# Performance work log

Hardware: AMD Instinct MI355X
Metric: run time of the kernel (lower is better)

## Reference

```python
import jax, jax.numpy as jnp
import numpy as np

N_NODES = 50000
N_EDGES = 800000
IN_F = 128
OUT_F = 128

def setup_inputs() -> dict:
    key = jax.random.key(0)
    k1, k2, k3, k4, k5, k6 = jax.random.split(key, 6)
    x = jax.random.normal(k1, (N_NODES, IN_F), dtype=jnp.float32)
    edge_row = jax.random.randint(k2, (N_EDGES,), 0, N_NODES, dtype=jnp.int32)
    edge_col = jax.random.randint(k3, (N_EDGES,), 0, N_NODES, dtype=jnp.int32)
    edge_val = jax.random.uniform(k4, (N_EDGES,), dtype=jnp.float32)
    stdv = 1.0 / np.sqrt(OUT_F)
    weight = jax.random.uniform(k5, (IN_F, OUT_F), minval=-stdv, maxval=stdv, dtype=jnp.float32)
    bias_param = jax.random.uniform(k6, (OUT_F,), minval=-stdv, maxval=stdv, dtype=jnp.float32)
    return {"x": x, "edge_row": edge_row, "edge_col": edge_col,
            "edge_val": edge_val, "weight": weight, "bias_param": bias_param}

def reference(x, edge_row, edge_col, edge_val, weight, bias_param):
    # support = X @ W  (dense GEMM)
    support = jnp.matmul(x, weight)                      # [N, out_f]
    # out = spmm(adj, support): gather source rows, scale by edge value,
    # scatter-add into destination rows (COO SpMM)
    msgs = edge_val[:, None] * support[edge_col]         # [E, out_f]
    out = jax.ops.segment_sum(msgs, edge_row, num_segments=N_NODES)
    return out + bias_param
```

## Files before the change

kernel.cpp:

```cpp
#include <hip/hip_runtime.h>

#define IN_F 128
#define OUT_F 128
#define BROWS 64
#define BCAP  2048
#define CHUNK 4096
#define NBMAX 1024

typedef __attribute__((ext_vector_type(8))) short short8;
typedef __attribute__((ext_vector_type(4))) float floatx4;

__device__ __forceinline__ short f2bf(float f) {
  union { float f; unsigned u; } v; v.f = f;
  unsigned u = v.u;
  unsigned r = (u + 0x7fffu + ((u >> 16) & 1u)) >> 16;
  return (short)r;
}
__device__ __forceinline__ float bflo(unsigned u) { return __uint_as_float(u << 16); }
__device__ __forceinline__ float bfhi(unsigned u) { return __uint_as_float(u & 0xffff0000u); }

__global__ __launch_bounds__(256) void prep_all(const float* __restrict__ w,
                                                short* __restrict__ wt,
                                                int* __restrict__ cursor, int nb) {
  int i = blockIdx.x * 256 + threadIdx.x;
  int n = i >> 7, k = i & 127;
  wt[i] = f2bf(w[k * 128 + n]);
  if (i < nb) cursor[i] = i * BCAP;
}

__global__ __launch_bounds__(256) void gemm_bin(const float* __restrict__ x,
                                                const short* __restrict__ wt,
                                                unsigned short* __restrict__ sup,
                                                const int* __restrict__ erow,
                                                const int* __restrict__ ecol,
                                                const float* __restrict__ eval_,
                                                int* __restrict__ cursor,
                                                int2* __restrict__ slab,
                                                int n_nodes, int n_edges,
                                                int nb, int n_tiles) {
  __shared__ __align__(16) unsigned short stile[4][16 * 136];
  __shared__ int lhist[NBMAX];
  const int t = threadIdx.x;

  if ((int)blockIdx.x < n_tiles) {
    const int wv   = t >> 6;
    const int lane = t & 63;
    const int m    = lane & 15;
    const int q    = lane >> 4;
    const int row  = blockIdx.x * 64 + wv * 16 + m;

    floatx4 acc[8];
#pragma unroll
    for (int k = 0; k < 8; ++k) acc[k] = (floatx4)(0.f);

#pragma unroll
    for (int kk = 0; kk < 4; ++kk) {
      short8 a;
      if (row < n_nodes) {
        const float4* px = (const float4*)(x + (size_t)row * IN_F + kk * 32 + q * 8);
        float4 lo = px[0], hi = px[1];
        a[0] = f2bf(lo.x); a[1] = f2bf(lo.y); a[2] = f2bf(lo.z); a[3] = f2bf(lo.w);
        a[4] = f2bf(hi.x); a[5] = f2bf(hi.y); a[6] = f2bf(hi.z); a[7] = f2bf(hi.w);
      } else {
        a = (short8)(0);
      }
#pragma unroll
      for (int k = 0; k < 8; ++k) {
        short8 b = *(const short8*)(wt + (size_t)(16 * k + m) * 128 + kk * 32 + q * 8);
        acc[k] = __builtin_amdgcn_mfma_f32_16x16x32_bf16(a, b, acc[k], 0, 0, 0);
      }
    }
#pragma unroll
    for (int r = 0; r < 4; ++r)
#pragma unroll
      for (int k = 0; k < 8; ++k)
        stile[wv][(q * 4 + r) * 136 + 16 * k + m] = (unsigned short)f2bf(acc[k][r]);
#pragma unroll
    for (int p = 0; p < 4; ++p) {
      int row_l = p * 4 + (lane >> 4);
      int row_g = blockIdx.x * 64 + wv * 16 + row_l;
      if (row_g < n_nodes) {
        uint4 v = *(const uint4*)&stile[wv][row_l * 136 + (lane & 15) * 8];
        *(uint4*)(sup + (size_t)row_g * OUT_F + (lane & 15) * 8) = v;
      }
    }
  } else {
    for (int b = t; b < nb; b += 256) lhist[b] = 0;
    __syncthreads();

    const int base = (blockIdx.x - n_tiles) * CHUNK;
    int meta[16], col[16]; float val[16];
#pragma unroll
    for (int i = 0; i < 16; ++i) {
      int e = base + i * 256 + t;
      meta[i] = -1;
      if (e < n_edges) {
        int r  = erow[e];
        col[i] = ecol[e];
        val[i] = eval_[e];
        int bk = r >> 6, rl = r & 63;
        int rank = atomicAdd(&lhist[bk], 1);
        meta[i] = (bk << 18) | (rl << 12) | rank;
      }
    }
    __syncthreads();
    for (int bk = t; bk < nb; bk += 256) {
      int c = lhist[bk];
      lhist[bk] = c ? atomicAdd(&cursor[bk], c) : 0;
    }
    __syncthreads();
#pragma unroll
    for (int i = 0; i < 16; ++i) {
      if (meta[i] >= 0) {
        int bk = meta[i] >> 18, rl = (meta[i] >> 12) & 63, rank = meta[i] & 0xfff;
        int pos = lhist[bk] + rank;
        if (pos < (bk + 1) * BCAP)
          slab[pos] = make_int2(col[i] | (rl << 16), __float_as_int(val[i]));
      }
    }
  }
}

__global__ __launch_bounds__(256) void spmm_sorted(const int* __restrict__ cursor,
                                                   const int2* __restrict__ slab,
                                                   const uint4* __restrict__ supv,
                                                   const float* __restrict__ bias,
                                                   float* __restrict__ out,
                                                   int n_nodes) {
  __shared__ int2 srec[BCAP];
  __shared__ int  roff[BROWS + 1];
  __shared__ int  rcur[BROWS];
  const int t = threadIdx.x, b = blockIdx.x;
  const int start = b * BCAP;
  const int cnt = min(cursor[b] - start, BCAP);
  const int wv = t >> 6, lane = t & 63;

  if (t < BROWS) rcur[t] = 0;
  __syncthreads();
  for (int i = t; i < cnt; i += 256)
    atomicAdd(&rcur[(slab[start + i].x >> 16) & 63], 1);
  __syncthreads();
  if (wv == 0) {
    int c = rcur[lane];
    int inc = c;
#pragma unroll
    for (int d = 1; d < 64; d <<= 1) {
      int u = __shfl_up(inc, d);
      if (lane >= d) inc += u;
    }
    roff[lane + 1] = inc;
    if (lane == 0) roff[0] = 0;
  }
  __syncthreads();
  if (t < BROWS) rcur[t] = roff[t];
  __syncthreads();
  for (int i = t; i < cnt; i += 256) {
    int2 r = slab[start + i];
    int p = atomicAdd(&rcur[(r.x >> 16) & 63], 1);
    srec[p] = r;
  }
  __syncthreads();

  const int g = lane >> 4, s = lane & 15;
  const float4* bp = (const float4*)bias + s * 2;
  const float4 b0 = bp[0], b1 = bp[1];

#pragma unroll
  for (int it = 0; it < 4; ++it) {
    const int rl = it * 16 + wv * 4 + g;
    const int s0 = roff[rl];
    const int c  = roff[rl + 1] - s0;
    int mx = max(c, __shfl_xor(c, 16));
    mx = max(mx, __shfl_xor(mx, 32));

    float a0 = 0.f, a1 = 0.f, a2 = 0.f, a3 = 0.f,
          a4 = 0.f, a5 = 0.f, a6 = 0.f, a7 = 0.f;

    int2  rec[4];
    uint4 sv[4];
#pragma unroll
    for (int k = 0; k < 4; ++k)
      rec[k] = (k < c) ? srec[s0 + k] : make_int2(0, 0);
#pragma unroll
    for (int k = 0; k < 4; ++k)
      sv[k] = supv[(size_t)(rec[k].x & 0xffff) * 16 + s];

    for (int j = 0; j < mx; j += 4) {
#pragma unroll
      for (int k = 0; k < 4; ++k) {
        const int jj = j + k;
        int2 recn = (jj + 4 < c) ? srec[s0 + jj + 4] : make_int2(0, 0);
        uint4 svn = supv[(size_t)(recn.x & 0xffff) * 16 + s];
        float v = (jj < c) ? __int_as_float(rec[k].y) : 0.f;
        a0 = fmaf(v, bflo(sv[k].x), a0);
        a1 = fmaf(v, bfhi(sv[k].x), a1);
        a2 = fmaf(v, bflo(sv[k].y), a2);
        a3 = fmaf(v, bfhi(sv[k].y), a3);
        a4 = fmaf(v, bflo(sv[k].z), a4);
        a5 = fmaf(v, bfhi(sv[k].z), a5);
        a6 = fmaf(v, bflo(sv[k].w), a6);
        a7 = fmaf(v, bfhi(sv[k].w), a7);
        rec[k] = recn; sv[k] = svn;
      }
    }

    const int row = b * BROWS + rl;
    if (row < n_nodes) {
      float4* op = (float4*)(out + (size_t)row * OUT_F + s * 8);
      op[0] = make_float4(a0 + b0.x, a1 + b0.y, a2 + b0.z, a3 + b0.w);
      op[1] = make_float4(a4 + b1.x, a5 + b1.y, a6 + b1.z, a7 + b1.w);
    }
  }
}

extern "C" void kernel_launch(void* const* d_in, const int* in_sizes, int n_in,
                              void* d_out, int out_size, void* d_ws, size_t ws_size,
                              hipStream_t stream) {
  const float* x     = (const float*)d_in[0];
  const int*   erow  = (const int*)d_in[1];
  const int*   ecol  = (const int*)d_in[2];
  const float* eval_ = (const float*)d_in[3];
  const float* w     = (const float*)d_in[4];
  const float* bias  = (const float*)d_in[5];
  float* out = (float*)d_out;

  const int n_nodes  = in_sizes[0] / IN_F;
  const int n_edges  = in_sizes[1];
  const int nb       = (n_nodes + BROWS - 1) / BROWS;
  const int n_tiles  = (n_nodes + 63) / 64;
  const int n_chunks = (n_edges + CHUNK - 1) / CHUNK;

  char* ws = (char*)d_ws;
  size_t off = 0;
  auto carve = [&](size_t bytes) { void* p = ws + off; off = (off + bytes + 255) & ~(size_t)255; return p; };
  unsigned short* sup = (unsigned short*)carve((size_t)n_nodes * OUT_F * sizeof(unsigned short));
  short* wt           = (short*)carve((size_t)IN_F * OUT_F * sizeof(short));
  int*   cursor       = (int*)  carve((size_t)nb * sizeof(int));
  int2*  slab         = (int2*) carve((size_t)nb * BCAP * sizeof(int2));

  prep_all<<<64, 256, 0, stream>>>(w, wt, cursor, nb);
  gemm_bin<<<n_tiles + n_chunks, 256, 0, stream>>>(x, wt, sup, erow, ecol, eval_,
                                                   cursor, slab, n_nodes, n_edges,
                                                   nb, n_tiles);
  spmm_sorted<<<nb, 256, 0, stream>>>(cursor, slab, (const uint4*)sup, bias, out, n_nodes);
}
```

Baseline: 138.4 us.

## Balance edge work across row groups via merge-path split in SpMM block

Each 16-lane group used to own fixed rows, so a wave's loop ran to the longest row among its groups. Now each of the 16 groups in the block takes an equal slice of the block's sorted edges, found by binary search over the row offsets. It walks those edges in order and flushes a row's result whenever a row boundary is crossed. This evens out load imbalance from varying row degrees, but adds data-dependent branches inside the inner loop and divergence within each wave.

```diff
diff --git a/kernel.cpp b/kernel.cpp
--- a/kernel.cpp
+++ b/kernel.cpp
@@ -161,17 +161,32 @@
   }
   __syncthreads();
 
-  const int g = lane >> 4, s = lane & 15;
+  const int gid = t >> 4;
+  const int s   = t & 15;
   const float4* bp = (const float4*)bias + s * 2;
   const float4 b0 = bp[0], b1 = bp[1];
-
-#pragma unroll
-  for (int it = 0; it < 4; ++it) {
-    const int rl = it * 16 + wv * 4 + g;
-    const int s0 = roff[rl];
-    const int c  = roff[rl + 1] - s0;
-    int mx = max(c, __shfl_xor(c, 16));
-    mx = max(mx, __shfl_xor(mx, 32));
+  const int row0 = b * BROWS;
+
+  int ra, rb;
+  {
+    int tgt = (gid * cnt) >> 4;
+    int lo = 0, hi = 64;
+    while (lo < hi) { int m = (lo + hi) >> 1; if (roff[m] >= tgt) hi = m; else lo = m + 1; }
+    ra = lo;
+    if (gid == 15) rb = 64;
+    else {
+      tgt = ((gid + 1) * cnt) >> 4;
+      lo = 0; hi = 64;
+      while (lo < hi) { int m = (lo + hi) >> 1; if (roff[m] >= tgt) hi = m; else lo = m + 1; }
+      rb = lo;
+    }
+  }
+
+  if (ra < rb) {
+    const int j0 = roff[ra];
+    const int j1 = roff[rb];
+    int cur  = ra;
+    int nend = roff[cur + 1];
 
     float a0 = 0.f, a1 = 0.f, a2 = 0.f, a3 = 0.f,
           a4 = 0.f, a5 = 0.f, a6 = 0.f, a7 = 0.f;
@@ -180,35 +195,49 @@
     uint4 sv[4];
 #pragma unroll
     for (int k = 0; k < 4; ++k)
-      rec[k] = (k < c) ? srec[s0 + k] : make_int2(0, 0);
+      rec[k] = (j0 + k < j1) ? srec[j0 + k] : make_int2(0, 0);
 #pragma unroll
     for (int k = 0; k < 4; ++k)
       sv[k] = supv[(size_t)(rec[k].x & 0xffff) * 16 + s];
 
-    for (int j = 0; j < mx; j += 4) {
+    for (int jb = j0; jb < j1; jb += 4) {
 #pragma unroll
       for (int k = 0; k < 4; ++k) {
-        const int jj = j + k;
-        int2 recn = (jj + 4 < c) ? srec[s0 + jj + 4] : make_int2(0, 0);
-        uint4 svn = supv[(size_t)(recn.x & 0xffff) * 16 + s];
-        float v = (jj < c) ? __int_as_float(rec[k].y) : 0.f;
-        a0 = fmaf(v, bflo(sv[k].x), a0);
-        a1 = fmaf(v, bfhi(sv[k].x), a1);
-        a2 = fmaf(v, bflo(sv[k].y), a2);
-        a3 = fmaf(v, bfhi(sv[k].y), a3);
-        a4 = fmaf(v, bflo(sv[k].z), a4);
-        a5 = fmaf(v, bfhi(sv[k].z), a5);
-        a6 = fmaf(v, bflo(sv[k].w), a6);
-        a7 = fmaf(v, bfhi(sv[k].w), a7);
-        rec[k] = recn; sv[k] = svn;
-      }
-    }
-
-    const int row = b * BROWS + rl;
-    if (row < n_nodes) {
-      float4* op = (float4*)(out + (size_t)row * OUT_F + s * 8);
-      op[0] = make_float4(a0 + b0.x, a1 + b0.y, a2 + b0.z, a3 + b0.w);
-      op[1] = make_float4(a4 + b1.x, a5 + b1.y, a6 + b1.z, a7 + b1.w);
+        const int jj = jb + k;
+        if (jj < j1) {
+          while (jj == nend) {
+            if (row0 + cur < n_nodes) {
+              float4* op = (float4*)(out + (size_t)(row0 + cur) * OUT_F + s * 8);
+              op[0] = make_float4(a0 + b0.x, a1 + b0.y, a2 + b0.z, a3 + b0.w);
+              op[1] = make_float4(a4 + b1.x, a5 + b1.y, a6 + b1.z, a7 + b1.w);
+            }
+            a0 = a1 = a2 = a3 = a4 = a5 = a6 = a7 = 0.f;
+            ++cur;
+            nend = roff[cur + 1];
+          }
+          float v = __int_as_float(rec[k].y);
+          a0 = fmaf(v, bflo(sv[k].x), a0);
+          a1 = fmaf(v, bfhi(sv[k].x), a1);
+          a2 = fmaf(v, bflo(sv[k].y), a2);
+          a3 = fmaf(v, bfhi(sv[k].y), a3);
+          a4 = fmaf(v, bflo(sv[k].z), a4);
+          a5 = fmaf(v, bfhi(sv[k].z), a5);
+          a6 = fmaf(v, bflo(sv[k].w), a6);
+          a7 = fmaf(v, bfhi(sv[k].w), a7);
+          int2 recn = (jj + 4 < j1) ? srec[jj + 4] : make_int2(0, 0);
+          rec[k] = recn;
+          sv[k] = supv[(size_t)(recn.x & 0xffff) * 16 + s];
+        }
+      }
+    }
+    while (cur < rb) {
+      if (row0 + cur < n_nodes) {
+        float4* op = (float4*)(out + (size_t)(row0 + cur) * OUT_F + s * 8);
+        op[0] = make_float4(a0 + b0.x, a1 + b0.y, a2 + b0.z, a3 + b0.w);
+        op[1] = make_float4(a4 + b1.x, a5 + b1.y, a6 + b1.z, a7 + b1.w);
+      }
+      a0 = a1 = a2 = a3 = a4 = a5 = a6 = a7 = 0.f;
+      ++cur;
     }
   }
 }
```

After: 138.7 us, median of 2. No clear change (+0.2%).
